# Kernel optimization log

Hardware: AMD Instinct MI355X
Metric: run time of the kernel (lower is better)

The kernel has to match this reference:

```python
import jax, jax.numpy as jnp
import numpy as np

B, S, HID, NH = 2, 2048, 2048, 16
ROPE, NOPE, VDIM = 64, 64, 128
QHEAD = ROPE + NOPE            # 128
QLORA = HID // 3               # 682
KVLORA = HID // 8              # 256
THETA = 128000.0
SCALE = 1.0 / np.sqrt(QHEAD)   # deepseek softmax_scale = q_head_dim**-0.5
EPS = 1e-6


def rmsnorm(x, w):
    var = jnp.mean(x.astype(jnp.float32) ** 2, axis=-1, keepdims=True)
    return (x.astype(jnp.float32) * jax.lax.rsqrt(var + EPS)).astype(x.dtype) * w


def rope_cos_sin(seq, dim, theta):
    inv = 1.0 / (theta ** (jnp.arange(0, dim, 2, dtype=jnp.float32) / dim))
    t = jnp.arange(seq, dtype=jnp.float32)
    freqs = jnp.outer(t, inv)                      # [S, dim/2]
    emb = jnp.concatenate([freqs, freqs], axis=-1)  # [S, dim]
    return jnp.cos(emb), jnp.sin(emb)


def apply_rope(x, cos, sin):
    # deepseek interleave: view(b,h,s,d/2,2).transpose(-1,-2).reshape, then rotate_half rope
    b, h, s, d = x.shape
    x = x.reshape(b, h, s, d // 2, 2).transpose(0, 1, 2, 4, 3).reshape(b, h, s, d)
    x1, x2 = jnp.split(x, 2, axis=-1)
    rot = jnp.concatenate([-x2, x1], axis=-1)
    return x * cos + rot * sin


def setup_inputs() -> dict:
    key = jax.random.key(0)
    ks = jax.random.split(key, 8)
    s = lambda fan_in: 1.0 / np.sqrt(fan_in)
    return {
        "x":        jax.random.normal(ks[0], (B, S, HID), jnp.float32),
        "q_a_w":    jax.random.normal(ks[1], (HID, QLORA), jnp.float32) * s(HID),
        "q_a_ln_w": jnp.ones((QLORA,), jnp.float32),
        "q_b_w":    jax.random.normal(ks[2], (QLORA, NH * QHEAD), jnp.float32) * s(QLORA),
        "kv_a_w":   jax.random.normal(ks[3], (HID, KVLORA + ROPE), jnp.float32) * s(HID),
        "kv_a_ln_w": jnp.ones((KVLORA,), jnp.float32),
        "kv_b_w":   jax.random.normal(ks[4], (KVLORA, NH * (NOPE + VDIM)), jnp.float32) * s(KVLORA),
        "o_w":      jax.random.normal(ks[5], (NH * VDIM, HID), jnp.float32) * s(NH * VDIM),
    }


def reference(x, q_a_w, q_a_ln_w, q_b_w, kv_a_w, kv_a_ln_w, kv_b_w, o_w):
    b, s, _ = x.shape
    # Q: low-rank down-proj -> RMSNorm -> up-proj
    q = rmsnorm(x @ q_a_w, q_a_ln_w) @ q_b_w               # [b,s,NH*QHEAD]
    q = q.reshape(b, s, NH, QHEAD).transpose(0, 2, 1, 3)   # [b,NH,s,QHEAD]
    q_nope, q_pe = q[..., :NOPE], q[..., NOPE:]
    # KV: compressed latent + shared rope key
    ckv_kpe = x @ kv_a_w                                   # [b,s,KVLORA+ROPE]
    ckv, k_pe = ckv_kpe[..., :KVLORA], ckv_kpe[..., KVLORA:]
    k_pe = k_pe.reshape(b, 1, s, ROPE)                     # shared across heads
    kv = rmsnorm(ckv, kv_a_ln_w) @ kv_b_w                  # [b,s,NH*(NOPE+VDIM)]
    kv = kv.reshape(b, s, NH, NOPE + VDIM).transpose(0, 2, 1, 3)
    k_nope, v = kv[..., :NOPE], kv[..., NOPE:]             # [b,NH,s,NOPE], [b,NH,s,VDIM]
    # decoupled RoPE on the rope split only
    cos, sin = rope_cos_sin(s, ROPE, THETA)
    q_pe = apply_rope(q_pe, cos, sin)
    k_pe = apply_rope(k_pe, cos, sin)
    qf = jnp.concatenate([q_nope, q_pe], axis=-1)          # [b,NH,s,QHEAD]
    kf = jnp.concatenate([k_nope, jnp.broadcast_to(k_pe, (b, NH, s, ROPE))], axis=-1)
    scores = jnp.einsum('bhqd,bhkd->bhqk', qf, kf) * SCALE
    causal = jnp.tril(jnp.ones((s, s), bool))
    scores = jnp.where(causal, scores, jnp.float32(-1e9))
    attn = jax.nn.softmax(scores.astype(jnp.float32), axis=-1).astype(qf.dtype)
    out = jnp.einsum('bhqk,bhkd->bhqd', attn, v)           # [b,NH,s,VDIM]
    out = out.transpose(0, 2, 1, 3).reshape(b, s, NH * VDIM)
    return out @ o_w                                       # [b,s,HID]
```

## Files before the change

### kernel.cpp

```cpp
#include <hip/hip_runtime.h>
#include <hip/hip_bf16.h>

typedef __attribute__((ext_vector_type(8))) short short8;
typedef __attribute__((ext_vector_type(4))) float f32x4;

using bf16 = __hip_bfloat16;

static constexpr int B_ = 2, S_ = 2048, HID_ = 2048, NH_ = 16;
static constexpr int ROPE_ = 64, VDIM_ = 128, QHEAD_ = 128;
static constexpr int QLORA_ = 682, KVLORA_ = 256;
static constexpr int QLORA_P = 704;
static constexpr int NQA_P = 768;
static constexpr int NKVA_P = 384;
static constexpr int NA_ = NQA_P + NKVA_P;
static constexpr float THETA_ = 128000.0f;
static constexpr float SCALE_ = 0.08838834764831845f;
static constexpr float SCL2_ = 0.08838834764831845f * 1.4426950408889634f;
static constexpr float EPS_ = 1e-6f;
static constexpr int BS_ = B_ * S_;

__device__ __forceinline__ void gl2lds16(const void* g, void* l) {
    __builtin_amdgcn_global_load_lds(
        (const __attribute__((address_space(1))) unsigned int*)g,
        (__attribute__((address_space(3))) unsigned int*)l, 16, 0, 0);
}

struct bf16x4_s { bf16 x, y, z, w; };

__device__ __forceinline__ float bfLo(unsigned int u) { return __uint_as_float(u << 16); }
__device__ __forceinline__ float bfHi(unsigned int u) { return __uint_as_float(u & 0xffff0000u); }

struct TD { const float* src; bf16* dst; const float* colw;
            int Ksrc, Nsrc, Kpad, tilesX, off, perm; };
struct TDs { TD d[5]; };
static constexpr int PREP_TILES = 8576;

__global__ void k_prep(TDs P, const float* __restrict__ x, bf16* __restrict__ xb,
                       float* __restrict__ ct, float* __restrict__ st) {
    __shared__ float tile[32][33];
    if (blockIdx.x >= PREP_TILES) {
        int bid = blockIdx.x - PREP_TILES;
        int t = threadIdx.y * 32 + threadIdx.x;
        if (bid < 8192) {
            int i = bid * 256 + t;
            float4 v = reinterpret_cast<const float4*>(x)[i];
            bf16x4_s o;
            o.x = __float2bfloat16(v.x); o.y = __float2bfloat16(v.y);
            o.z = __float2bfloat16(v.z); o.w = __float2bfloat16(v.w);
            reinterpret_cast<bf16x4_s*>(xb)[i] = o;
        } else {
            int idx = (bid - 8192) * 256 + t;
            int tpos = idx >> 5, j = idx & 31;
            float inv = expf(-(float)j * (logf(THETA_) / 32.0f));
            float f = (float)tpos * inv;
            ct[idx] = cosf(f);
            st[idx] = sinf(f);
        }
        return;
    }
    int flat = blockIdx.x;
    int di = 0;
    #pragma unroll
    for (int i = 1; i < 5; ++i) if (flat >= P.d[i].off) di = i;
    TD d = P.d[di];
    int local = flat - d.off;
    int xt = local % d.tilesX, yt = local / d.tilesX;
    int kb = xt * 32, nb = yt * 32;
    int tx = threadIdx.x, ty = threadIdx.y;
    #pragma unroll
    for (int i = 0; i < 32; i += 8) {
        int k = kb + ty + i, n = nb + tx;
        float v = (k < d.Ksrc && n < d.Nsrc) ? d.src[(size_t)k * d.Nsrc + n] : 0.0f;
        if (d.colw && k < d.Ksrc) v *= d.colw[k];
        tile[ty + i][tx] = v;
    }
    __syncthreads();
    int u = ty * 32 + tx;
    int kp = u & 15;
    int nl = u >> 4;
    #pragma unroll
    for (int half = 0; half < 2; ++half) {
        int n_loc = nl + 16 * half;
        int n = nb + n_loc;
        int nd = n;
        if (d.perm) {
            int h = n / 192, dd = n - h * 192;
            nd = (dd < 64) ? h * 64 + dd : 1024 + h * 128 + (dd - 64);
        }
        bf16 lo = __float2bfloat16(tile[2 * kp][n_loc]);
        bf16 hi = __float2bfloat16(tile[2 * kp + 1][n_loc]);
        unsigned int pk = (unsigned int)*reinterpret_cast<unsigned short*>(&lo) |
                          ((unsigned int)*reinterpret_cast<unsigned short*>(&hi) << 16);
        *reinterpret_cast<unsigned int*>(d.dst + (size_t)nd * d.Kpad + kb + 2 * kp) = pk;
    }
}

#define GEMM_VARS                                                                        \
    __shared__ bf16 As[128 * 64];                                                        \
    __shared__ bf16 Bs[128 * 64];                                                        \
    const int t = threadIdx.x;                                                           \
    const int lane = t & 63, w = t >> 6;                                                 \
    const int l15 = lane & 15, l4 = lane >> 4;                                           \
    const int wr = (w >> 1) * 64, wc = (w & 1) * 64;

#define GEMM_CORE(Aptr, Bptr, LDA, LDB, KDIM, M0V, N0V)                                  \
    const int m0 = (M0V), n0 = (N0V);                                                    \
    f32x4 acc[4][4] = {};                                                                \
    for (int k0 = 0; k0 < (KDIM); k0 += 64) {                                            \
        _Pragma("unroll")                                                                \
        for (int i = 0; i < 4; ++i) {                                                    \
            int cid = t + i * 256;                                                       \
            int row = cid >> 3;                                                          \
            int ch = (cid & 7) ^ (row & 7);                                              \
            gl2lds16((Aptr) + (size_t)(m0 + row) * (LDA) + k0 + ch * 8,                  \
                     reinterpret_cast<char*>(As) + cid * 16);                            \
            gl2lds16((Bptr) + (size_t)(n0 + row) * (LDB) + k0 + ch * 8,                  \
                     reinterpret_cast<char*>(Bs) + cid * 16);                            \
        }                                                                                \
        __syncthreads();                                                                 \
        _Pragma("unroll")                                                                \
        for (int kk = 0; kk < 2; ++kk) {                                                 \
            short8 a[4], b[4];                                                           \
            _Pragma("unroll")                                                            \
            for (int m = 0; m < 4; ++m) {                                                \
                int row = wr + m * 16 + l15;                                             \
                int ch = (kk * 4 + l4) ^ (row & 7);                                      \
                a[m] = *reinterpret_cast<const short8*>(                                 \
                    reinterpret_cast<const char*>(As) + row * 128 + ch * 16);            \
            }                                                                            \
            _Pragma("unroll")                                                            \
            for (int n = 0; n < 4; ++n) {                                                \
                int row = wc + n * 16 + l15;                                             \
                int ch = (kk * 4 + l4) ^ (row & 7);                                      \
                b[n] = *reinterpret_cast<const short8*>(                                 \
                    reinterpret_cast<const char*>(Bs) + row * 128 + ch * 16);            \
            }                                                                            \
            _Pragma("unroll")                                                            \
            for (int m = 0; m < 4; ++m)                                                  \
                _Pragma("unroll")                                                        \
                for (int n = 0; n < 4; ++n)                                              \
                    acc[m][n] = __builtin_amdgcn_mfma_f32_16x16x32_bf16(a[m], b[n],      \
                                                                       acc[m][n], 0, 0, 0); \
        }                                                                                \
        __syncthreads();                                                                 \
    }

template <typename OutT>
__launch_bounds__(256)
__global__ void gemm_bt(const bf16* __restrict__ A, const bf16* __restrict__ Bt,
                        OutT* __restrict__ C, int K, int lda, int ldb, int ldc)
{
    GEMM_VARS
    GEMM_CORE(A, Bt, lda, ldb, K, blockIdx.y * 128, blockIdx.x * 128)
    #pragma unroll
    for (int m = 0; m < 4; ++m)
        #pragma unroll
        for (int n = 0; n < 4; ++n)
            #pragma unroll
            for (int j = 0; j < 4; ++j) {
                int r = m0 + wr + m * 16 + l4 * 4 + j;
                int c = n0 + wc + n * 16 + l15;
                float v = acc[m][n][j];
                if constexpr (sizeof(OutT) == 2) C[(size_t)r * ldc + c] = __float2bfloat16(v);
                else                             C[(size_t)r * ldc + c] = v;
            }
}

__launch_bounds__(256)
__global__ void gemm_up(const bf16* __restrict__ qac, const bf16* __restrict__ qb_wt,
                        const float* __restrict__ ct, const float* __restrict__ st,
                        const float* __restrict__ qs, bf16* __restrict__ Qf,
                        const bf16* __restrict__ kvb_wt, const float* __restrict__ ks,
                        bf16* __restrict__ knope, bf16* __restrict__ Vt)
{
    GEMM_VARS
    if (blockIdx.x < 16) {
        GEMM_CORE(qac, qb_wt, NA_, QLORA_P, QLORA_P, blockIdx.y * 128, blockIdx.x * 128)
        (void)n0;
        const int h = blockIdx.x;
        if (wc == 0) {
            #pragma unroll
            for (int m = 0; m < 4; ++m) {
                int rb = m0 + wr + m * 16 + l4 * 4;
                float q4[4];
                #pragma unroll
                for (int j = 0; j < 4; ++j) q4[j] = qs[rb + j] * SCL2_;
                #pragma unroll
                for (int n = 0; n < 4; ++n)
                    #pragma unroll
                    for (int j = 0; j < 4; ++j) {
                        int r = rb + j;
                        int c = n * 16 + l15;
                        int s = r & (S_ - 1), bq = r >> 11;
                        Qf[((size_t)(bq * NH_ + h) * S_ + s) * 128 + c] =
                            __float2bfloat16(acc[m][n][j] * q4[j]);
                    }
            }
        } else {
            #pragma unroll
            for (int m = 0; m < 4; ++m) {
                int rb = m0 + wr + m * 16 + l4 * 4;
                float q4[4];
                #pragma unroll
                for (int j = 0; j < 4; ++j) q4[j] = qs[rb + j] * SCL2_;
                #pragma unroll
                for (int n = 0; n < 4; ++n)
                    #pragma unroll
                    for (int j = 0; j < 4; ++j) {
                        int r = rb + j;
                        int p = n * 16 + l15;
                        int jj = p >> 1, odd = p & 1;
                        float v = acc[m][n][j];
                        float pr = __shfl_xor(v, 1);
                        float e0 = odd ? pr : v, e1 = odd ? v : pr;
                        int s = r & (S_ - 1), bq = r >> 11;
                        float c_ = ct[s * 32 + jj], s_ = st[s * 32 + jj];
                        float ov = odd ? (e1 * c_ + e0 * s_) : (e0 * c_ - e1 * s_);
                        int c_out = 64 + (odd ? 32 : 0) + jj;
                        Qf[((size_t)(bq * NH_ + h) * S_ + s) * 128 + c_out] =
                            __float2bfloat16(ov * q4[j]);
                    }
            }
        }
    } else {
        GEMM_CORE(qac + NQA_P, kvb_wt, NA_, KVLORA_, KVLORA_, blockIdx.y * 128,
                  (blockIdx.x - 16) * 128)
        if (n0 < 1024) {
            #pragma unroll
            for (int m = 0; m < 4; ++m) {
                int rb = m0 + wr + m * 16 + l4 * 4;
                float k4[4];
                #pragma unroll
                for (int j = 0; j < 4; ++j) k4[j] = ks[rb + j];
                #pragma unroll
                for (int n = 0; n < 4; ++n)
                    #pragma unroll
                    for (int j = 0; j < 4; ++j) {
                        int c = n0 + wc + n * 16 + l15;
                        knope[(size_t)(rb + j) * 1024 + c] =
                            __float2bfloat16(acc[m][n][j] * k4[j]);
                    }
            }
        } else {
            const int h = (n0 - 1024) >> 7;
            const int bq = m0 >> 11;
            const int bh = bq * NH_ + h;
            #pragma unroll
            for (int m = 0; m < 4; ++m) {
                int rb = m0 + wr + m * 16 + l4 * 4;
                int s = rb & (S_ - 1);
                float k4[4];
                #pragma unroll
                for (int j = 0; j < 4; ++j) k4[j] = ks[rb + j];
                #pragma unroll
                for (int n = 0; n < 4; ++n) {
                    int cl = wc + n * 16 + l15;
                    ushort4 pk;
                    {
                        bf16 h0 = __float2bfloat16(acc[m][n][0] * k4[0]);
                        bf16 h1 = __float2bfloat16(acc[m][n][1] * k4[1]);
                        bf16 h2 = __float2bfloat16(acc[m][n][2] * k4[2]);
                        bf16 h3 = __float2bfloat16(acc[m][n][3] * k4[3]);
                        pk.x = *reinterpret_cast<unsigned short*>(&h0);
                        pk.y = *reinterpret_cast<unsigned short*>(&h1);
                        pk.z = *reinterpret_cast<unsigned short*>(&h2);
                        pk.w = *reinterpret_cast<unsigned short*>(&h3);
                    }
                    *reinterpret_cast<ushort4*>(Vt + ((size_t)bh * 128 + cl) * S_ + s) = pk;
                }
            }
        }
    }
}

__launch_bounds__(256)
__global__ void k_scales(const bf16* __restrict__ qac,
                         const float* __restrict__ ct, const float* __restrict__ st,
                         float* __restrict__ qs, float* __restrict__ ks,
                         bf16* __restrict__ kr)
{
    __shared__ float red[8];
    int bs = blockIdx.x;
    int t = threadIdx.x, lane = t & 63, w = t >> 6;
    int s = bs & (S_ - 1);
    const unsigned int* qp = reinterpret_cast<const unsigned int*>(qac + (size_t)bs * NA_);
    float sq = 0.f, sk = 0.f;
    for (int p = t; p < 341; p += 256) {
        unsigned int u = qp[p];
        float a = bfLo(u), b = bfHi(u);
        sq += a * a + b * b;
    }
    if (t < 128) {
        unsigned int u = qp[384 + t];
        float a = bfLo(u), b = bfHi(u);
        sk = a * a + b * b;
    }
    #pragma unroll
    for (int m = 1; m < 64; m <<= 1) { sq += __shfl_xor(sq, m); sk += __shfl_xor(sk, m); }
    if (lane == 0) { red[w] = sq; red[4 + w] = sk; }
    __syncthreads();
    if (t == 0) {
        sq = red[0] + red[1] + red[2] + red[3];
        sk = red[4] + red[5] + red[6] + red[7];
        qs[bs] = rsqrtf(sq / (float)QLORA_ + EPS_);
        ks[bs] = rsqrtf(sk / (float)KVLORA_ + EPS_);
    }
    if (t < 64) {
        int j = t & 31;
        float c_ = ct[s * 32 + j], s_ = st[s * 32 + j];
        unsigned int u = qp[512 + j];
        float e0 = bfLo(u), e1 = bfHi(u);
        float v = (t < 32) ? (e0 * c_ - e1 * s_) : (e1 * c_ + e0 * s_);
        kr[(size_t)bs * 64 + t] = __float2bfloat16(v);
    }
}

__launch_bounds__(512, 4)
__global__ void k_flash(const bf16* __restrict__ Qf, const bf16* __restrict__ knope,
                        const bf16* __restrict__ kr, const bf16* __restrict__ Vt,
                        bf16* __restrict__ attn_out)
{
    __shared__ bf16 Ks[2][64 * 128];
    __shared__ bf16 Vs[2][128 * 64];
    __shared__ bf16 Ps[8][16 * 64];

    const int t = threadIdx.x, lane = t & 63, w = t >> 6;
    const int l15 = lane & 15, l4 = lane >> 4;
    const int pi = blockIdx.y;
    const int bh = blockIdx.x;
    const int b = bh >> 4, h = bh & 15;
    const int strip = (w < 4) ? (31 - pi) : pi;
    const int r0 = strip * 64 + (w & 3) * 16;
    const int NT = 32 - pi;

    short8 qa_[4];
    {
        const bf16* qrow = Qf + ((size_t)bh * S_ + r0 + l15) * 128;
        #pragma unroll
        for (int kk = 0; kk < 4; ++kk)
            qa_[kk] = *reinterpret_cast<const short8*>(qrow + kk * 32 + l4 * 8);
    }

    const bf16 *kSrc0, *kSrc1, *vSrc0, *vSrc1;
    size_t kStp0, kStp1;
    {
        int cid = t, row = cid >> 4, ch = (cid & 15) ^ (row & 7);
        kSrc0 = (ch < 8) ? knope + (size_t)(b * S_ + row) * 1024 + h * 64 + ch * 8
                         : kr + (size_t)(b * S_ + row) * 64 + (ch - 8) * 8;
        kStp0 = (ch < 8) ? (size_t)64 * 1024 : (size_t)64 * 64;
    }
    {
        int cid = t + 512, row = cid >> 4, ch = (cid & 15) ^ (row & 7);
        kSrc1 = (ch < 8) ? knope + (size_t)(b * S_ + row) * 1024 + h * 64 + ch * 8
                         : kr + (size_t)(b * S_ + row) * 64 + (ch - 8) * 8;
        kStp1 = (ch < 8) ? (size_t)64 * 1024 : (size_t)64 * 64;
    }
    {
        const bf16* Vg = Vt + (size_t)bh * 128 * S_;
        int cid = t, row = cid >> 3, ch = (cid & 7) ^ (row & 7);
        vSrc0 = Vg + (size_t)row * S_ + ch * 8;
        cid = t + 512; row = cid >> 3; ch = (cid & 7) ^ (row & 7);
        vSrc1 = Vg + (size_t)row * S_ + ch * 8;
    }
    auto stage = [&](int buf) {
        gl2lds16(kSrc0, reinterpret_cast<char*>(Ks[buf]) + t * 16);
        gl2lds16(kSrc1, reinterpret_cast<char*>(Ks[buf]) + (t + 512) * 16);
        gl2lds16(vSrc0, reinterpret_cast<char*>(Vs[buf]) + t * 16);
        gl2lds16(vSrc1, reinterpret_cast<char*>(Vs[buf]) + (t + 512) * 16);
        kSrc0 += kStp0; kSrc1 += kStp1; vSrc0 += 64; vSrc1 += 64;
    };

    stage(0);
    __syncthreads();

    f32x4 o[8] = {};
    float m_r = -1e30f, l_r = 0.f;

    int cur = 0;
    for (int kb = 0; kb < NT; ++kb) {
        const int k0 = kb * 64;
        if (kb + 1 < NT) stage(cur ^ 1);

        if (k0 <= r0 + 15) {
            f32x4 sfr[4] = {};
            __builtin_amdgcn_s_setprio(1);
            #pragma unroll
            for (int kk = 0; kk < 4; ++kk) {
                short8 kf[4];
                #pragma unroll
                for (int m = 0; m < 4; ++m) {
                    int row = m * 16 + l15;
                    int ch = (kk * 4 + l4) ^ (row & 7);
                    kf[m] = *reinterpret_cast<const short8*>(
                        reinterpret_cast<const char*>(Ks[cur]) + row * 256 + ch * 16);
                }
                #pragma unroll
                for (int m = 0; m < 4; ++m)
                    sfr[m] = __builtin_amdgcn_mfma_f32_16x16x32_bf16(kf[m], qa_[kk], sfr[m], 0, 0, 0);
            }
            __builtin_amdgcn_s_setprio(0);

            const int qrow = r0 + l15;
            if (k0 + 63 > r0) {
                #pragma unroll
                for (int m = 0; m < 4; ++m) {
                    int kbase = k0 + m * 16 + l4 * 4;
                    #pragma unroll
                    for (int j = 0; j < 4; ++j)
                        if (kbase + j > qrow) sfr[m][j] = -1e30f;
                }
            }

            float rm;
            {
                float a0 = fmaxf(fmaxf(sfr[0][0], sfr[0][1]), fmaxf(sfr[0][2], sfr[0][3]));
                float a1 = fmaxf(fmaxf(sfr[1][0], sfr[1][1]), fmaxf(sfr[1][2], sfr[1][3]));
                float a2 = fmaxf(fmaxf(sfr[2][0], sfr[2][1]), fmaxf(sfr[2][2], sfr[2][3]));
                float a3 = fmaxf(fmaxf(sfr[3][0], sfr[3][1]), fmaxf(sfr[3][2], sfr[3][3]));
                rm = fmaxf(fmaxf(a0, a1), fmaxf(a2, a3));
            }
            rm = fmaxf(rm, __shfl_xor(rm, 16));
            rm = fmaxf(rm, __shfl_xor(rm, 32));

            if (__ballot(rm > m_r + 8.0f)) {
                float mn = fmaxf(m_r, rm);
                float alpha = exp2f(m_r - mn);
                m_r = mn;
                l_r *= alpha;
                float aj[4];
                #pragma unroll
                for (int j = 0; j < 4; ++j) aj[j] = __shfl(alpha, l4 * 4 + j);
                #pragma unroll
                for (int n = 0; n < 8; ++n)
                    #pragma unroll
                    for (int j = 0; j < 4; ++j) o[n][j] *= aj[j];
            }

            char* pb = reinterpret_cast<char*>(Ps[w]);
            float rs = 0.f;
            #pragma unroll
            for (int m = 0; m < 4; ++m) {
                float p0 = exp2f(sfr[m][0] - m_r);
                float p1 = exp2f(sfr[m][1] - m_r);
                float p2 = exp2f(sfr[m][2] - m_r);
                float p3 = exp2f(sfr[m][3] - m_r);
                rs += (p0 + p1) + (p2 + p3);
                union { __hip_bfloat162 h; unsigned int u; } cl, ch2;
                cl.h  = __float22bfloat162_rn(make_float2(p0, p1));
                ch2.h = __float22bfloat162_rn(make_float2(p2, p3));
                int kloc = m * 16 + l4 * 4;
                int chnk = (kloc >> 3) ^ (l15 & 7);
                uint2 pk2; pk2.x = cl.u; pk2.y = ch2.u;
                *reinterpret_cast<uint2*>(pb + l15 * 128 + chnk * 16 + (kloc & 7) * 2) = pk2;
            }
            rs += __shfl_xor(rs, 16);
            rs += __shfl_xor(rs, 32);
            l_r += rs;

            __builtin_amdgcn_s_setprio(1);
            #pragma unroll
            for (int kk = 0; kk < 2; ++kk) {
                int pch = (kk * 4 + l4) ^ (l15 & 7);
                short8 pa = *reinterpret_cast<const short8*>(pb + l15 * 128 + pch * 16);
                #pragma unroll
                for (int n = 0; n < 8; ++n) {
                    int row = n * 16 + l15;
                    int ch = (kk * 4 + l4) ^ (row & 7);
                    short8 vb = *reinterpret_cast<const short8*>(
                        reinterpret_cast<const char*>(Vs[cur]) + row * 128 + ch * 16);
                    o[n] = __builtin_amdgcn_mfma_f32_16x16x32_bf16(pa, vb, o[n], 0, 0, 0);
                }
            }
            __builtin_amdgcn_s_setprio(0);
        }
        __syncthreads();
        cur ^= 1;
    }

    float rj[4];
    #pragma unroll
    for (int j = 0; j < 4; ++j) rj[j] = __builtin_amdgcn_rcpf(__shfl(l_r, l4 * 4 + j));
    size_t obase = ((size_t)(b * S_) + r0) * (size_t)(NH_ * VDIM_) + h * VDIM_;
    #pragma unroll
    for (int n = 0; n < 8; ++n)
        #pragma unroll
        for (int j = 0; j < 4; ++j) {
            int r = l4 * 4 + j;
            int c = n * 16 + l15;
            attn_out[obase + (size_t)r * (NH_ * VDIM_) + c] = __float2bfloat16(o[n][j] * rj[j]);
        }
}

extern "C" void kernel_launch(void* const* d_in, const int* in_sizes, int n_in,
                              void* d_out, int out_size, void* d_ws, size_t ws_size,
                              hipStream_t stream)
{
    (void)in_sizes; (void)n_in; (void)out_size;
    const float* x       = (const float*)d_in[0];
    const float* q_a_w   = (const float*)d_in[1];
    const float* q_a_ln  = (const float*)d_in[2];
    const float* q_b_w   = (const float*)d_in[3];
    const float* kv_a_w  = (const float*)d_in[4];
    const float* kv_a_ln = (const float*)d_in[5];
    const float* kv_b_w  = (const float*)d_in[6];
    const float* o_w     = (const float*)d_in[7];
    float* out = (float*)d_out;

    char* ws = (char*)d_ws;
    size_t off = 0;
    auto alloc = [&](size_t bytes) -> char* {
        char* p = ws + off;
        off += (bytes + 255) & ~(size_t)255;
        return p;
    };

    bf16* xb     = (bf16*)alloc((size_t)BS_ * HID_ * 2);
    bf16* a_wt   = (bf16*)alloc((size_t)NA_ * HID_ * 2);
    bf16* qb_wt  = (bf16*)alloc((size_t)2048 * QLORA_P * 2);
    bf16* kvb_wt = (bf16*)alloc((size_t)3072 * KVLORA_ * 2);
    bf16* ow_t   = (bf16*)alloc((size_t)2048 * 2048 * 2);
    float* ct    = (float*)alloc((size_t)S_ * 32 * 4);
    float* st    = (float*)alloc((size_t)S_ * 32 * 4);
    bf16* qac    = (bf16*)alloc((size_t)BS_ * NA_ * 2);
    float* qs    = (float*)alloc((size_t)BS_ * 4);
    float* ksc   = (float*)alloc((size_t)BS_ * 4);
    bf16* kr     = (bf16*)alloc((size_t)BS_ * 64 * 2);
    bf16* knope  = (bf16*)alloc((size_t)BS_ * 1024 * 2);
    bf16* Vt     = (bf16*)alloc((size_t)BS_ * 2048 * 2);
    bf16* attn   = (bf16*)alloc((size_t)BS_ * 2048 * 2);

    bf16* Qf = xb;

    if (ws_size < off) return;

    TDs P;
    P.d[0] = TD{ q_a_w,  a_wt,                     nullptr, 2048,  682, 2048, 64,    0, 0 };
    P.d[1] = TD{ kv_a_w, a_wt + (size_t)NQA_P*2048,nullptr, 2048,  320, 2048, 64, 1536, 0 };
    P.d[2] = TD{ q_b_w,  qb_wt,                    q_a_ln,   682, 2048,  704, 22, 2304, 0 };
    P.d[3] = TD{ kv_b_w, kvb_wt,                   kv_a_ln,  256, 3072,  256,  8, 3712, 1 };
    P.d[4] = TD{ o_w,    ow_t,                     nullptr, 2048, 2048, 2048, 64, 4480, 0 };
    k_prep<<<PREP_TILES + 8192 + 256, dim3(32, 8), 0, stream>>>(P, x, xb, ct, st);

    gemm_bt<bf16><<<dim3(NA_ / 128, BS_ / 128), 256, 0, stream>>>(xb, a_wt, qac,
                                                                  HID_, HID_, HID_, NA_);

    k_scales<<<BS_, 256, 0, stream>>>(qac, ct, st, qs, ksc, kr);

    gemm_up<<<dim3(16 + 24, BS_ / 128), 256, 0, stream>>>(qac, qb_wt, ct, st, qs, Qf,
                                                          kvb_wt, ksc, knope, Vt);

    k_flash<<<dim3(B_ * NH_, 16), 512, 0, stream>>>(Qf, knope, kr, Vt, attn);

    gemm_bt<float><<<dim3(2048 / 128, BS_ / 128), 256, 0, stream>>>(attn, ow_t, out,
                                                                    HID_, HID_, HID_, 2048);
}
```

Baseline: 220.0 us.

## Fuse RMS sum-of-squares and k_pe RoPE into down-proj GEMM epilogue; single-buffer flash LDS

The down-projection GEMM epilogue now accumulates per-row sums of squares with atomics into zeroed buffers and applies RoPE to the k_pe columns. This removes the separate k_scales kernel and its re-read of qac. The up-projection computes rsqrt from these sums. Separately, the flash kernel drops K/V double buffering in favor of a single LDS buffer, which lowers LDS use (possibly raising occupancy) but loses overlap of loads with compute. Atomic float sums also make the normalization nondeterministic in rounding.

```diff
diff --git a/kernel.cpp b/kernel.cpp
--- a/kernel.cpp
+++ b/kernel.cpp
@@ -36,7 +36,8 @@
 static constexpr int PREP_TILES = 8576;
 
 __global__ void k_prep(TDs P, const float* __restrict__ x, bf16* __restrict__ xb,
-                       float* __restrict__ ct, float* __restrict__ st) {
+                       float* __restrict__ ct, float* __restrict__ st,
+                       float* __restrict__ sums) {
     __shared__ float tile[32][33];
     if (blockIdx.x >= PREP_TILES) {
         int bid = blockIdx.x - PREP_TILES;
@@ -48,13 +49,16 @@
             o.x = __float2bfloat16(v.x); o.y = __float2bfloat16(v.y);
             o.z = __float2bfloat16(v.z); o.w = __float2bfloat16(v.w);
             reinterpret_cast<bf16x4_s*>(xb)[i] = o;
-        } else {
+        } else if (bid < 8192 + 256) {
             int idx = (bid - 8192) * 256 + t;
             int tpos = idx >> 5, j = idx & 31;
             float inv = expf(-(float)j * (logf(THETA_) / 32.0f));
             float f = (float)tpos * inv;
             ct[idx] = cosf(f);
             st[idx] = sinf(f);
+        } else {
+            int z = bid - (8192 + 256);
+            reinterpret_cast<float4*>(sums)[z * 256 + t] = make_float4(0.f, 0.f, 0.f, 0.f);
         }
         return;
     }
@@ -167,10 +171,62 @@
 }
 
 __launch_bounds__(256)
+__global__ void gemm_a(const bf16* __restrict__ A, const bf16* __restrict__ Bt,
+                       bf16* __restrict__ qac,
+                       const float* __restrict__ ct, const float* __restrict__ st,
+                       float* __restrict__ qsum, float* __restrict__ ksum,
+                       bf16* __restrict__ kr)
+{
+    GEMM_VARS
+    GEMM_CORE(A, Bt, HID_, HID_, HID_, blockIdx.y * 128, blockIdx.x * 128)
+    if (n0 < 1024) {
+        #pragma unroll
+        for (int m = 0; m < 4; ++m)
+            #pragma unroll
+            for (int n = 0; n < 4; ++n)
+                #pragma unroll
+                for (int j = 0; j < 4; ++j) {
+                    int r = m0 + wr + m * 16 + l4 * 4 + j;
+                    int c = n0 + wc + n * 16 + l15;
+                    qac[(size_t)r * NA_ + c] = __float2bfloat16(acc[m][n][j]);
+                }
+        float* dst = (n0 < 768) ? qsum : ksum;
+        #pragma unroll
+        for (int m = 0; m < 4; ++m)
+            #pragma unroll
+            for (int j = 0; j < 4; ++j) {
+                float v = acc[m][0][j] * acc[m][0][j] + acc[m][1][j] * acc[m][1][j]
+                        + acc[m][2][j] * acc[m][2][j] + acc[m][3][j] * acc[m][3][j];
+                v += __shfl_xor(v, 1); v += __shfl_xor(v, 2);
+                v += __shfl_xor(v, 4); v += __shfl_xor(v, 8);
+                if (l15 == 0) atomicAdd(&dst[m0 + wr + m * 16 + l4 * 4 + j], v);
+            }
+    } else if (wc == 0) {
+        #pragma unroll
+        for (int m = 0; m < 4; ++m)
+            #pragma unroll
+            for (int n = 0; n < 4; ++n)
+                #pragma unroll
+                for (int j = 0; j < 4; ++j) {
+                    int r = m0 + wr + m * 16 + l4 * 4 + j;
+                    int p = n * 16 + l15;
+                    int jj = p >> 1, odd = p & 1;
+                    float v = acc[m][n][j];
+                    float pr = __shfl_xor(v, 1);
+                    float e0 = odd ? pr : v, e1 = odd ? v : pr;
+                    int s = r & (S_ - 1);
+                    float c_ = ct[s * 32 + jj], s_ = st[s * 32 + jj];
+                    float ov = odd ? (e1 * c_ + e0 * s_) : (e0 * c_ - e1 * s_);
+                    kr[(size_t)r * 64 + (odd ? 32 : 0) + jj] = __float2bfloat16(ov);
+                }
+    }
+}
+
+__launch_bounds__(256)
 __global__ void gemm_up(const bf16* __restrict__ qac, const bf16* __restrict__ qb_wt,
                         const float* __restrict__ ct, const float* __restrict__ st,
-                        const float* __restrict__ qs, bf16* __restrict__ Qf,
-                        const bf16* __restrict__ kvb_wt, const float* __restrict__ ks,
+                        const float* __restrict__ qsum, bf16* __restrict__ Qf,
+                        const bf16* __restrict__ kvb_wt, const float* __restrict__ ksum,
                         bf16* __restrict__ knope, bf16* __restrict__ Vt)
 {
     GEMM_VARS
@@ -184,7 +240,8 @@
                 int rb = m0 + wr + m * 16 + l4 * 4;
                 float q4[4];
                 #pragma unroll
-                for (int j = 0; j < 4; ++j) q4[j] = qs[rb + j] * SCL2_;
+                for (int j = 0; j < 4; ++j)
+                    q4[j] = rsqrtf(qsum[rb + j] * (1.0f / (float)QLORA_) + EPS_) * SCL2_;
                 #pragma unroll
                 for (int n = 0; n < 4; ++n)
                     #pragma unroll
@@ -202,7 +259,8 @@
                 int rb = m0 + wr + m * 16 + l4 * 4;
                 float q4[4];
                 #pragma unroll
-                for (int j = 0; j < 4; ++j) q4[j] = qs[rb + j] * SCL2_;
+                for (int j = 0; j < 4; ++j)
+                    q4[j] = rsqrtf(qsum[rb + j] * (1.0f / (float)QLORA_) + EPS_) * SCL2_;
                 #pragma unroll
                 for (int n = 0; n < 4; ++n)
                     #pragma unroll
@@ -231,7 +289,8 @@
                 int rb = m0 + wr + m * 16 + l4 * 4;
                 float k4[4];
                 #pragma unroll
-                for (int j = 0; j < 4; ++j) k4[j] = ks[rb + j];
+                for (int j = 0; j < 4; ++j)
+                    k4[j] = rsqrtf(ksum[rb + j] * (1.0f / (float)KVLORA_) + EPS_);
                 #pragma unroll
                 for (int n = 0; n < 4; ++n)
                     #pragma unroll
@@ -251,7 +310,8 @@
                 int s = rb & (S_ - 1);
                 float k4[4];
                 #pragma unroll
-                for (int j = 0; j < 4; ++j) k4[j] = ks[rb + j];
+                for (int j = 0; j < 4; ++j)
+                    k4[j] = rsqrtf(ksum[rb + j] * (1.0f / (float)KVLORA_) + EPS_);
                 #pragma unroll
                 for (int n = 0; n < 4; ++n) {
                     int cl = wc + n * 16 + l15;
@@ -273,55 +333,13 @@
     }
 }
 
-__launch_bounds__(256)
-__global__ void k_scales(const bf16* __restrict__ qac,
-                         const float* __restrict__ ct, const float* __restrict__ st,
-                         float* __restrict__ qs, float* __restrict__ ks,
-                         bf16* __restrict__ kr)
-{
-    __shared__ float red[8];
-    int bs = blockIdx.x;
-    int t = threadIdx.x, lane = t & 63, w = t >> 6;
-    int s = bs & (S_ - 1);
-    const unsigned int* qp = reinterpret_cast<const unsigned int*>(qac + (size_t)bs * NA_);
-    float sq = 0.f, sk = 0.f;
-    for (int p = t; p < 341; p += 256) {
-        unsigned int u = qp[p];
-        float a = bfLo(u), b = bfHi(u);
-        sq += a * a + b * b;
-    }
-    if (t < 128) {
-        unsigned int u = qp[384 + t];
-        float a = bfLo(u), b = bfHi(u);
-        sk = a * a + b * b;
-    }
-    #pragma unroll
-    for (int m = 1; m < 64; m <<= 1) { sq += __shfl_xor(sq, m); sk += __shfl_xor(sk, m); }
-    if (lane == 0) { red[w] = sq; red[4 + w] = sk; }
-    __syncthreads();
-    if (t == 0) {
-        sq = red[0] + red[1] + red[2] + red[3];
-        sk = red[4] + red[5] + red[6] + red[7];
-        qs[bs] = rsqrtf(sq / (float)QLORA_ + EPS_);
-        ks[bs] = rsqrtf(sk / (float)KVLORA_ + EPS_);
-    }
-    if (t < 64) {
-        int j = t & 31;
-        float c_ = ct[s * 32 + j], s_ = st[s * 32 + j];
-        unsigned int u = qp[512 + j];
-        float e0 = bfLo(u), e1 = bfHi(u);
-        float v = (t < 32) ? (e0 * c_ - e1 * s_) : (e1 * c_ + e0 * s_);
-        kr[(size_t)bs * 64 + t] = __float2bfloat16(v);
-    }
-}
-
 __launch_bounds__(512, 4)
 __global__ void k_flash(const bf16* __restrict__ Qf, const bf16* __restrict__ knope,
                         const bf16* __restrict__ kr, const bf16* __restrict__ Vt,
                         bf16* __restrict__ attn_out)
 {
-    __shared__ bf16 Ks[2][64 * 128];
-    __shared__ bf16 Vs[2][128 * 64];
+    __shared__ bf16 Ks[64 * 128];
+    __shared__ bf16 Vs[128 * 64];
     __shared__ bf16 Ps[8][16 * 64];
 
     const int t = threadIdx.x, lane = t & 63, w = t >> 6;
@@ -362,24 +380,22 @@
         cid = t + 512; row = cid >> 3; ch = (cid & 7) ^ (row & 7);
         vSrc1 = Vg + (size_t)row * S_ + ch * 8;
     }
-    auto stage = [&](int buf) {
-        gl2lds16(kSrc0, reinterpret_cast<char*>(Ks[buf]) + t * 16);
-        gl2lds16(kSrc1, reinterpret_cast<char*>(Ks[buf]) + (t + 512) * 16);
-        gl2lds16(vSrc0, reinterpret_cast<char*>(Vs[buf]) + t * 16);
-        gl2lds16(vSrc1, reinterpret_cast<char*>(Vs[buf]) + (t + 512) * 16);
+    auto stage = [&]() {
+        gl2lds16(kSrc0, reinterpret_cast<char*>(Ks) + t * 16);
+        gl2lds16(kSrc1, reinterpret_cast<char*>(Ks) + (t + 512) * 16);
+        gl2lds16(vSrc0, reinterpret_cast<char*>(Vs) + t * 16);
+        gl2lds16(vSrc1, reinterpret_cast<char*>(Vs) + (t + 512) * 16);
         kSrc0 += kStp0; kSrc1 += kStp1; vSrc0 += 64; vSrc1 += 64;
     };
 
-    stage(0);
-    __syncthreads();
+    stage();
 
     f32x4 o[8] = {};
     float m_r = -1e30f, l_r = 0.f;
 
-    int cur = 0;
     for (int kb = 0; kb < NT; ++kb) {
         const int k0 = kb * 64;
-        if (kb + 1 < NT) stage(cur ^ 1);
+        __syncthreads();
 
         if (k0 <= r0 + 15) {
             f32x4 sfr[4] = {};
@@ -392,7 +408,7 @@
                     int row = m * 16 + l15;
                     int ch = (kk * 4 + l4) ^ (row & 7);
                     kf[m] = *reinterpret_cast<const short8*>(
-                        reinterpret_cast<const char*>(Ks[cur]) + row * 256 + ch * 16);
+                        reinterpret_cast<const char*>(Ks) + row * 256 + ch * 16);
                 }
                 #pragma unroll
                 for (int m = 0; m < 4; ++m)
@@ -467,14 +483,14 @@
                     int row = n * 16 + l15;
                     int ch = (kk * 4 + l4) ^ (row & 7);
                     short8 vb = *reinterpret_cast<const short8*>(
-                        reinterpret_cast<const char*>(Vs[cur]) + row * 128 + ch * 16);
+                        reinterpret_cast<const char*>(Vs) + row * 128 + ch * 16);
                     o[n] = __builtin_amdgcn_mfma_f32_16x16x32_bf16(pa, vb, o[n], 0, 0, 0);
                 }
             }
             __builtin_amdgcn_s_setprio(0);
         }
         __syncthreads();
-        cur ^= 1;
+        if (kb + 1 < NT) stage();
     }
 
     float rj[4];
@@ -522,8 +538,8 @@
     float* ct    = (float*)alloc((size_t)S_ * 32 * 4);
     float* st    = (float*)alloc((size_t)S_ * 32 * 4);
     bf16* qac    = (bf16*)alloc((size_t)BS_ * NA_ * 2);
-    float* qs    = (float*)alloc((size_t)BS_ * 4);
-    float* ksc   = (float*)alloc((size_t)BS_ * 4);
+    float* qsum  = (float*)alloc((size_t)8192 * 4);
+    float* ksum  = qsum + BS_;
     bf16* kr     = (bf16*)alloc((size_t)BS_ * 64 * 2);
     bf16* knope  = (bf16*)alloc((size_t)BS_ * 1024 * 2);
     bf16* Vt     = (bf16*)alloc((size_t)BS_ * 2048 * 2);
@@ -539,15 +555,13 @@
     P.d[2] = TD{ q_b_w,  qb_wt,                    q_a_ln,   682, 2048,  704, 22, 2304, 0 };
     P.d[3] = TD{ kv_b_w, kvb_wt,                   kv_a_ln,  256, 3072,  256,  8, 3712, 1 };
     P.d[4] = TD{ o_w,    ow_t,                     nullptr, 2048, 2048, 2048, 64, 4480, 0 };
-    k_prep<<<PREP_TILES + 8192 + 256, dim3(32, 8), 0, stream>>>(P, x, xb, ct, st);
-
-    gemm_bt<bf16><<<dim3(NA_ / 128, BS_ / 128), 256, 0, stream>>>(xb, a_wt, qac,
-                                                                  HID_, HID_, HID_, NA_);
-
-    k_scales<<<BS_, 256, 0, stream>>>(qac, ct, st, qs, ksc, kr);
-
-    gemm_up<<<dim3(16 + 24, BS_ / 128), 256, 0, stream>>>(qac, qb_wt, ct, st, qs, Qf,
-                                                          kvb_wt, ksc, knope, Vt);
+    k_prep<<<PREP_TILES + 8192 + 256 + 8, dim3(32, 8), 0, stream>>>(P, x, xb, ct, st, qsum);
+
+    gemm_a<<<dim3(NA_ / 128, BS_ / 128), 256, 0, stream>>>(xb, a_wt, qac, ct, st,
+                                                           qsum, ksum, kr);
+
+    gemm_up<<<dim3(16 + 24, BS_ / 128), 256, 0, stream>>>(qac, qb_wt, ct, st, qsum, Qf,
+                                                          kvb_wt, ksum, knope, Vt);
 
     k_flash<<<dim3(B_ * NH_, 16), 512, 0, stream>>>(Qf, knope, kr, Vt, attn);
 
```

New measurement: 216.7 us. About the same (-1.5%).

## Fuse k_pe RoPE into down-proj GEMM epilogue and restructure flash grid

Applied to the files above, without the earlier changes.

The down-projection GEMM gets a custom epilogue that applies RoPE to the k_pe columns and writes kr directly, so k_scales no longer handles RoPE. The flash attention kernel drops the paired long/short strip scheme with 512 threads and double-buffered K/V. It now launches one 256-thread block per 64-row strip (32 per head) with a single LDS buffer and barriers around each stage. This lowers LDS use per block so more blocks can be resident, but it gives up the overlap of the next tile's load with compute and relies on the scheduler to balance the uneven causal strip lengths.

```diff
diff --git a/kernel.cpp b/kernel.cpp
--- a/kernel.cpp
+++ b/kernel.cpp
@@ -167,6 +167,77 @@
 }
 
 __launch_bounds__(256)
+__global__ void gemm_a(const bf16* __restrict__ A, const bf16* __restrict__ Bt,
+                       bf16* __restrict__ qac,
+                       const float* __restrict__ ct, const float* __restrict__ st,
+                       bf16* __restrict__ kr)
+{
+    GEMM_VARS
+    GEMM_CORE(A, Bt, HID_, HID_, HID_, blockIdx.y * 128, blockIdx.x * 128)
+    if (n0 < 1024) {
+        #pragma unroll
+        for (int m = 0; m < 4; ++m)
+            #pragma unroll
+            for (int n = 0; n < 4; ++n)
+                #pragma unroll
+                for (int j = 0; j < 4; ++j) {
+                    int r = m0 + wr + m * 16 + l4 * 4 + j;
+                    int c = n0 + wc + n * 16 + l15;
+                    qac[(size_t)r * NA_ + c] = __float2bfloat16(acc[m][n][j]);
+                }
+    } else if (wc == 0) {
+        #pragma unroll
+        for (int m = 0; m < 4; ++m)
+            #pragma unroll
+            for (int n = 0; n < 4; ++n)
+                #pragma unroll
+                for (int j = 0; j < 4; ++j) {
+                    int r = m0 + wr + m * 16 + l4 * 4 + j;
+                    int p = n * 16 + l15;
+                    int jj = p >> 1, odd = p & 1;
+                    float v = acc[m][n][j];
+                    float pr = __shfl_xor(v, 1);
+                    float e0 = odd ? pr : v, e1 = odd ? v : pr;
+                    int s = r & (S_ - 1);
+                    float c_ = ct[s * 32 + jj], s_ = st[s * 32 + jj];
+                    float ov = odd ? (e1 * c_ + e0 * s_) : (e0 * c_ - e1 * s_);
+                    kr[(size_t)r * 64 + (odd ? 32 : 0) + jj] = __float2bfloat16(ov);
+                }
+    }
+}
+
+__launch_bounds__(256)
+__global__ void k_scales(const bf16* __restrict__ qac,
+                         float* __restrict__ qs, float* __restrict__ ks)
+{
+    __shared__ float red[8];
+    int bs = blockIdx.x;
+    int t = threadIdx.x, lane = t & 63, w = t >> 6;
+    const unsigned int* qp = reinterpret_cast<const unsigned int*>(qac + (size_t)bs * NA_);
+    float sq = 0.f, sk = 0.f;
+    for (int p = t; p < 341; p += 256) {
+        unsigned int u = qp[p];
+        float a = bfLo(u), b = bfHi(u);
+        sq += a * a + b * b;
+    }
+    if (t < 128) {
+        unsigned int u = qp[384 + t];
+        float a = bfLo(u), b = bfHi(u);
+        sk = a * a + b * b;
+    }
+    #pragma unroll
+    for (int m = 1; m < 64; m <<= 1) { sq += __shfl_xor(sq, m); sk += __shfl_xor(sk, m); }
+    if (lane == 0) { red[w] = sq; red[4 + w] = sk; }
+    __syncthreads();
+    if (t == 0) {
+        sq = red[0] + red[1] + red[2] + red[3];
+        sk = red[4] + red[5] + red[6] + red[7];
+        qs[bs] = rsqrtf(sq / (float)QLORA_ + EPS_);
+        ks[bs] = rsqrtf(sk / (float)KVLORA_ + EPS_);
+    }
+}
+
+__launch_bounds__(256)
 __global__ void gemm_up(const bf16* __restrict__ qac, const bf16* __restrict__ qb_wt,
                         const float* __restrict__ ct, const float* __restrict__ st,
                         const float* __restrict__ qs, bf16* __restrict__ Qf,
@@ -273,65 +344,22 @@
     }
 }
 
-__launch_bounds__(256)
-__global__ void k_scales(const bf16* __restrict__ qac,
-                         const float* __restrict__ ct, const float* __restrict__ st,
-                         float* __restrict__ qs, float* __restrict__ ks,
-                         bf16* __restrict__ kr)
-{
-    __shared__ float red[8];
-    int bs = blockIdx.x;
-    int t = threadIdx.x, lane = t & 63, w = t >> 6;
-    int s = bs & (S_ - 1);
-    const unsigned int* qp = reinterpret_cast<const unsigned int*>(qac + (size_t)bs * NA_);
-    float sq = 0.f, sk = 0.f;
-    for (int p = t; p < 341; p += 256) {
-        unsigned int u = qp[p];
-        float a = bfLo(u), b = bfHi(u);
-        sq += a * a + b * b;
-    }
-    if (t < 128) {
-        unsigned int u = qp[384 + t];
-        float a = bfLo(u), b = bfHi(u);
-        sk = a * a + b * b;
-    }
-    #pragma unroll
-    for (int m = 1; m < 64; m <<= 1) { sq += __shfl_xor(sq, m); sk += __shfl_xor(sk, m); }
-    if (lane == 0) { red[w] = sq; red[4 + w] = sk; }
-    __syncthreads();
-    if (t == 0) {
-        sq = red[0] + red[1] + red[2] + red[3];
-        sk = red[4] + red[5] + red[6] + red[7];
-        qs[bs] = rsqrtf(sq / (float)QLORA_ + EPS_);
-        ks[bs] = rsqrtf(sk / (float)KVLORA_ + EPS_);
-    }
-    if (t < 64) {
-        int j = t & 31;
-        float c_ = ct[s * 32 + j], s_ = st[s * 32 + j];
-        unsigned int u = qp[512 + j];
-        float e0 = bfLo(u), e1 = bfHi(u);
-        float v = (t < 32) ? (e0 * c_ - e1 * s_) : (e1 * c_ + e0 * s_);
-        kr[(size_t)bs * 64 + t] = __float2bfloat16(v);
-    }
-}
-
-__launch_bounds__(512, 4)
+__launch_bounds__(256, 4)
 __global__ void k_flash(const bf16* __restrict__ Qf, const bf16* __restrict__ knope,
                         const bf16* __restrict__ kr, const bf16* __restrict__ Vt,
                         bf16* __restrict__ attn_out)
 {
-    __shared__ bf16 Ks[2][64 * 128];
-    __shared__ bf16 Vs[2][128 * 64];
-    __shared__ bf16 Ps[8][16 * 64];
+    __shared__ bf16 Ks[64 * 128];
+    __shared__ bf16 Vs[128 * 64];
+    __shared__ bf16 Ps[4][16 * 64];
 
     const int t = threadIdx.x, lane = t & 63, w = t >> 6;
     const int l15 = lane & 15, l4 = lane >> 4;
-    const int pi = blockIdx.y;
+    const int strip = 31 - blockIdx.y;
     const int bh = blockIdx.x;
     const int b = bh >> 4, h = bh & 15;
-    const int strip = (w < 4) ? (31 - pi) : pi;
-    const int r0 = strip * 64 + (w & 3) * 16;
-    const int NT = 32 - pi;
+    const int r0 = strip * 64 + w * 16;
+    const int NT = strip + 1;
 
     short8 qa_[4];
     {
@@ -341,140 +369,140 @@
             qa_[kk] = *reinterpret_cast<const short8*>(qrow + kk * 32 + l4 * 8);
     }
 
-    const bf16 *kSrc0, *kSrc1, *vSrc0, *vSrc1;
-    size_t kStp0, kStp1;
-    {
-        int cid = t, row = cid >> 4, ch = (cid & 15) ^ (row & 7);
-        kSrc0 = (ch < 8) ? knope + (size_t)(b * S_ + row) * 1024 + h * 64 + ch * 8
+    const bf16* kS[4]; size_t kStep[4];
+    const bf16* vS[4];
+    #pragma unroll
+    for (int i = 0; i < 4; ++i) {
+        int cid = t + i * 256;
+        int row = cid >> 4, ch = (cid & 15) ^ (row & 7);
+        kS[i] = (ch < 8) ? knope + (size_t)(b * S_ + row) * 1024 + h * 64 + ch * 8
                          : kr + (size_t)(b * S_ + row) * 64 + (ch - 8) * 8;
-        kStp0 = (ch < 8) ? (size_t)64 * 1024 : (size_t)64 * 64;
-    }
-    {
-        int cid = t + 512, row = cid >> 4, ch = (cid & 15) ^ (row & 7);
-        kSrc1 = (ch < 8) ? knope + (size_t)(b * S_ + row) * 1024 + h * 64 + ch * 8
-                         : kr + (size_t)(b * S_ + row) * 64 + (ch - 8) * 8;
-        kStp1 = (ch < 8) ? (size_t)64 * 1024 : (size_t)64 * 64;
+        kStep[i] = (ch < 8) ? (size_t)64 * 1024 : (size_t)64 * 64;
     }
     {
         const bf16* Vg = Vt + (size_t)bh * 128 * S_;
-        int cid = t, row = cid >> 3, ch = (cid & 7) ^ (row & 7);
-        vSrc0 = Vg + (size_t)row * S_ + ch * 8;
-        cid = t + 512; row = cid >> 3; ch = (cid & 7) ^ (row & 7);
-        vSrc1 = Vg + (size_t)row * S_ + ch * 8;
-    }
-    auto stage = [&](int buf) {
-        gl2lds16(kSrc0, reinterpret_cast<char*>(Ks[buf]) + t * 16);
-        gl2lds16(kSrc1, reinterpret_cast<char*>(Ks[buf]) + (t + 512) * 16);
-        gl2lds16(vSrc0, reinterpret_cast<char*>(Vs[buf]) + t * 16);
-        gl2lds16(vSrc1, reinterpret_cast<char*>(Vs[buf]) + (t + 512) * 16);
-        kSrc0 += kStp0; kSrc1 += kStp1; vSrc0 += 64; vSrc1 += 64;
+        #pragma unroll
+        for (int i = 0; i < 4; ++i) {
+            int cid = t + i * 256;
+            int row = cid >> 3, ch = (cid & 7) ^ (row & 7);
+            vS[i] = Vg + (size_t)row * S_ + ch * 8;
+        }
+    }
+    auto stage = [&]() {
+        #pragma unroll
+        for (int i = 0; i < 4; ++i) {
+            gl2lds16(kS[i], reinterpret_cast<char*>(Ks) + (t + i * 256) * 16);
+            kS[i] += kStep[i];
+        }
+        #pragma unroll
+        for (int i = 0; i < 4; ++i) {
+            gl2lds16(vS[i], reinterpret_cast<char*>(Vs) + (t + i * 256) * 16);
+            vS[i] += 64;
+        }
     };
 
-    stage(0);
-    __syncthreads();
+    stage();
 
     f32x4 o[8] = {};
     float m_r = -1e30f, l_r = 0.f;
 
-    int cur = 0;
     for (int kb = 0; kb < NT; ++kb) {
         const int k0 = kb * 64;
-        if (kb + 1 < NT) stage(cur ^ 1);
-
-        if (k0 <= r0 + 15) {
-            f32x4 sfr[4] = {};
-            __builtin_amdgcn_s_setprio(1);
-            #pragma unroll
-            for (int kk = 0; kk < 4; ++kk) {
-                short8 kf[4];
-                #pragma unroll
-                for (int m = 0; m < 4; ++m) {
-                    int row = m * 16 + l15;
-                    int ch = (kk * 4 + l4) ^ (row & 7);
-                    kf[m] = *reinterpret_cast<const short8*>(
-                        reinterpret_cast<const char*>(Ks[cur]) + row * 256 + ch * 16);
-                }
-                #pragma unroll
-                for (int m = 0; m < 4; ++m)
-                    sfr[m] = __builtin_amdgcn_mfma_f32_16x16x32_bf16(kf[m], qa_[kk], sfr[m], 0, 0, 0);
-            }
-            __builtin_amdgcn_s_setprio(0);
-
-            const int qrow = r0 + l15;
-            if (k0 + 63 > r0) {
-                #pragma unroll
-                for (int m = 0; m < 4; ++m) {
-                    int kbase = k0 + m * 16 + l4 * 4;
-                    #pragma unroll
-                    for (int j = 0; j < 4; ++j)
-                        if (kbase + j > qrow) sfr[m][j] = -1e30f;
-                }
-            }
-
-            float rm;
-            {
-                float a0 = fmaxf(fmaxf(sfr[0][0], sfr[0][1]), fmaxf(sfr[0][2], sfr[0][3]));
-                float a1 = fmaxf(fmaxf(sfr[1][0], sfr[1][1]), fmaxf(sfr[1][2], sfr[1][3]));
-                float a2 = fmaxf(fmaxf(sfr[2][0], sfr[2][1]), fmaxf(sfr[2][2], sfr[2][3]));
-                float a3 = fmaxf(fmaxf(sfr[3][0], sfr[3][1]), fmaxf(sfr[3][2], sfr[3][3]));
-                rm = fmaxf(fmaxf(a0, a1), fmaxf(a2, a3));
-            }
-            rm = fmaxf(rm, __shfl_xor(rm, 16));
-            rm = fmaxf(rm, __shfl_xor(rm, 32));
-
-            if (__ballot(rm > m_r + 8.0f)) {
-                float mn = fmaxf(m_r, rm);
-                float alpha = exp2f(m_r - mn);
-                m_r = mn;
-                l_r *= alpha;
-                float aj[4];
-                #pragma unroll
-                for (int j = 0; j < 4; ++j) aj[j] = __shfl(alpha, l4 * 4 + j);
-                #pragma unroll
-                for (int n = 0; n < 8; ++n)
-                    #pragma unroll
-                    for (int j = 0; j < 4; ++j) o[n][j] *= aj[j];
-            }
-
-            char* pb = reinterpret_cast<char*>(Ps[w]);
-            float rs = 0.f;
+        __syncthreads();
+
+        f32x4 sfr[4] = {};
+        __builtin_amdgcn_s_setprio(1);
+        #pragma unroll
+        for (int kk = 0; kk < 4; ++kk) {
+            short8 kf[4];
             #pragma unroll
             for (int m = 0; m < 4; ++m) {
-                float p0 = exp2f(sfr[m][0] - m_r);
-                float p1 = exp2f(sfr[m][1] - m_r);
-                float p2 = exp2f(sfr[m][2] - m_r);
-                float p3 = exp2f(sfr[m][3] - m_r);
-                rs += (p0 + p1) + (p2 + p3);
-                union { __hip_bfloat162 h; unsigned int u; } cl, ch2;
-                cl.h  = __float22bfloat162_rn(make_float2(p0, p1));
-                ch2.h = __float22bfloat162_rn(make_float2(p2, p3));
-                int kloc = m * 16 + l4 * 4;
-                int chnk = (kloc >> 3) ^ (l15 & 7);
-                uint2 pk2; pk2.x = cl.u; pk2.y = ch2.u;
-                *reinterpret_cast<uint2*>(pb + l15 * 128 + chnk * 16 + (kloc & 7) * 2) = pk2;
-            }
-            rs += __shfl_xor(rs, 16);
-            rs += __shfl_xor(rs, 32);
-            l_r += rs;
-
-            __builtin_amdgcn_s_setprio(1);
-            #pragma unroll
-            for (int kk = 0; kk < 2; ++kk) {
-                int pch = (kk * 4 + l4) ^ (l15 & 7);
-                short8 pa = *reinterpret_cast<const short8*>(pb + l15 * 128 + pch * 16);
-                #pragma unroll
-                for (int n = 0; n < 8; ++n) {
-                    int row = n * 16 + l15;
-                    int ch = (kk * 4 + l4) ^ (row & 7);
-                    short8 vb = *reinterpret_cast<const short8*>(
-                        reinterpret_cast<const char*>(Vs[cur]) + row * 128 + ch * 16);
-                    o[n] = __builtin_amdgcn_mfma_f32_16x16x32_bf16(pa, vb, o[n], 0, 0, 0);
-                }
-            }
-            __builtin_amdgcn_s_setprio(0);
-        }
+                int row = m * 16 + l15;
+                int ch = (kk * 4 + l4) ^ (row & 7);
+                kf[m] = *reinterpret_cast<const short8*>(
+                    reinterpret_cast<const char*>(Ks) + row * 256 + ch * 16);
+            }
+            #pragma unroll
+            for (int m = 0; m < 4; ++m)
+                sfr[m] = __builtin_amdgcn_mfma_f32_16x16x32_bf16(kf[m], qa_[kk], sfr[m], 0, 0, 0);
+        }
+        __builtin_amdgcn_s_setprio(0);
+
+        const int qrow = r0 + l15;
+        if (k0 + 63 > r0) {
+            #pragma unroll
+            for (int m = 0; m < 4; ++m) {
+                int kbase = k0 + m * 16 + l4 * 4;
+                #pragma unroll
+                for (int j = 0; j < 4; ++j)
+                    if (kbase + j > qrow) sfr[m][j] = -1e30f;
+            }
+        }
+
+        float rm;
+        {
+            float a0 = fmaxf(fmaxf(sfr[0][0], sfr[0][1]), fmaxf(sfr[0][2], sfr[0][3]));
+            float a1 = fmaxf(fmaxf(sfr[1][0], sfr[1][1]), fmaxf(sfr[1][2], sfr[1][3]));
+            float a2 = fmaxf(fmaxf(sfr[2][0], sfr[2][1]), fmaxf(sfr[2][2], sfr[2][3]));
+            float a3 = fmaxf(fmaxf(sfr[3][0], sfr[3][1]), fmaxf(sfr[3][2], sfr[3][3]));
+            rm = fmaxf(fmaxf(a0, a1), fmaxf(a2, a3));
+        }
+        rm = fmaxf(rm, __shfl_xor(rm, 16));
+        rm = fmaxf(rm, __shfl_xor(rm, 32));
+
+        if (__ballot(rm > m_r + 8.0f)) {
+            float mn = fmaxf(m_r, rm);
+            float alpha = exp2f(m_r - mn);
+            m_r = mn;
+            l_r *= alpha;
+            float aj[4];
+            #pragma unroll
+            for (int j = 0; j < 4; ++j) aj[j] = __shfl(alpha, l4 * 4 + j);
+            #pragma unroll
+            for (int n = 0; n < 8; ++n)
+                #pragma unroll
+                for (int j = 0; j < 4; ++j) o[n][j] *= aj[j];
+        }
+
+        char* pb = reinterpret_cast<char*>(Ps[w]);
+        float rs = 0.f;
+        #pragma unroll
+        for (int m = 0; m < 4; ++m) {
+            float p0 = exp2f(sfr[m][0] - m_r);
+            float p1 = exp2f(sfr[m][1] - m_r);
+            float p2 = exp2f(sfr[m][2] - m_r);
+            float p3 = exp2f(sfr[m][3] - m_r);
+            rs += (p0 + p1) + (p2 + p3);
+            union { __hip_bfloat162 h; unsigned int u; } cl, ch2;
+            cl.h  = __float22bfloat162_rn(make_float2(p0, p1));
+            ch2.h = __float22bfloat162_rn(make_float2(p2, p3));
+            int kloc = m * 16 + l4 * 4;
+            int chnk = (kloc >> 3) ^ (l15 & 7);
+            uint2 pk2; pk2.x = cl.u; pk2.y = ch2.u;
+            *reinterpret_cast<uint2*>(pb + l15 * 128 + chnk * 16 + (kloc & 7) * 2) = pk2;
+        }
+        rs += __shfl_xor(rs, 16);
+        rs += __shfl_xor(rs, 32);
+        l_r += rs;
+
+        __builtin_amdgcn_s_setprio(1);
+        #pragma unroll
+        for (int kk = 0; kk < 2; ++kk) {
+            int pch = (kk * 4 + l4) ^ (l15 & 7);
+            short8 pa = *reinterpret_cast<const short8*>(pb + l15 * 128 + pch * 16);
+            #pragma unroll
+            for (int n = 0; n < 8; ++n) {
+                int row = n * 16 + l15;
+                int ch = (kk * 4 + l4) ^ (row & 7);
+                short8 vb = *reinterpret_cast<const short8*>(
+                    reinterpret_cast<const char*>(Vs) + row * 128 + ch * 16);
+                o[n] = __builtin_amdgcn_mfma_f32_16x16x32_bf16(pa, vb, o[n], 0, 0, 0);
+            }
+        }
+        __builtin_amdgcn_s_setprio(0);
+
         __syncthreads();
-        cur ^= 1;
+        if (kb + 1 < NT) stage();
     }
 
     float rj[4];
@@ -541,15 +569,14 @@
     P.d[4] = TD{ o_w,    ow_t,                     nullptr, 2048, 2048, 2048, 64, 4480, 0 };
     k_prep<<<PREP_TILES + 8192 + 256, dim3(32, 8), 0, stream>>>(P, x, xb, ct, st);
 
-    gemm_bt<bf16><<<dim3(NA_ / 128, BS_ / 128), 256, 0, stream>>>(xb, a_wt, qac,
-                                                                  HID_, HID_, HID_, NA_);
-
-    k_scales<<<BS_, 256, 0, stream>>>(qac, ct, st, qs, ksc, kr);
+    gemm_a<<<dim3(NA_ / 128, BS_ / 128), 256, 0, stream>>>(xb, a_wt, qac, ct, st, kr);
+
+    k_scales<<<BS_, 256, 0, stream>>>(qac, qs, ksc);
 
     gemm_up<<<dim3(16 + 24, BS_ / 128), 256, 0, stream>>>(qac, qb_wt, ct, st, qs, Qf,
                                                           kvb_wt, ksc, knope, Vt);
 
-    k_flash<<<dim3(B_ * NH_, 16), 512, 0, stream>>>(Qf, knope, kr, Vt, attn);
+    k_flash<<<dim3(B_ * NH_, 32), 256, 0, stream>>>(Qf, knope, kr, Vt, attn);
 
     gemm_bt<float><<<dim3(2048 / 128, BS_ / 128), 256, 0, stream>>>(attn, ow_t, out,
                                                                     HID_, HID_, HID_, 2048);
```

Measured after the change: 223.1 us. About the same (+1.4%).
